# Performance work log

Measured on AMD Instinct MI355X. Metric: run time of the kernel, lower is better.

## Reference

```python
import jax, jax.numpy as jnp
import numpy as np

B = 8192          # batch
NUM_PROTOS = 10   # num_prototypes
NUM_CLASSES = 10
N_PATCHES = 14 * 14  # 196 non-overlapping 2x2 patches of a 28x28 image


def setup_inputs() -> dict:
    key = jax.random.key(0)
    k1, k2, k3 = jax.random.split(key, 3)
    x = jax.random.normal(k1, (B, 784), dtype=jnp.float32)
    prototypes = jax.random.normal(k2, (NUM_PROTOS, 4), dtype=jnp.float32)
    W = jax.random.normal(k3, (NUM_CLASSES, NUM_PROTOS * N_PATCHES), dtype=jnp.float32) * 0.02
    b = jnp.zeros((NUM_CLASSES,), dtype=jnp.float32)
    return {"x": x, "prototypes": prototypes, "W": W, "b": b}


def _features(x, prototypes):
    # x: (B, 784) -> non-overlapping 2x2 patches, row-major within each patch
    bsz = x.shape[0]
    img = x.reshape(bsz, 28, 28)
    patches = img.reshape(bsz, 14, 2, 14, 2).transpose(0, 1, 3, 2, 4).reshape(bsz, N_PATCHES, 4)
    # Quantum kernel: ansatz applies RY(x_i) then RY(-y_i) per wire on |0000>.
    # |0...0> amplitude factorizes over the 4 wires: prod_i cos((x_i - y_i)/2).
    diff = patches[:, :, None, :] - prototypes[None, None, :, :]   # (B, 196, P, 4)
    kern = jnp.abs(jnp.prod(jnp.cos(0.5 * diff), axis=-1))          # (B, 196, P)
    # torch stacks per-prototype then permutes to (B, P, 196) and flattens
    return kern.transpose(0, 2, 1).reshape(bsz, -1)                 # (B, P*196)


def reference(x, prototypes, W, b):
    feats = _features(x, prototypes)
    logits = feats @ W.T + b
    return jax.nn.log_softmax(logits, axis=-1)
```

## Files before the change

kernel.cpp:

```cpp
#include <hip/hip_runtime.h>
#include <math.h>

#define B_ROWS 8192
#define NPROTO 10
#define NCLS   10
#define NPATCH 196
#define WROW   (NPROTO * NPATCH)

#define PART_OFF  0
#define XS_STRIDE 113

typedef float v2f __attribute__((ext_vector_type(2)));

__global__ __launch_bounds__(256) void quanv_main(
    const float* __restrict__ x, const float* __restrict__ protos,
    const float* __restrict__ W, float* __restrict__ partial) {
  __shared__ float xs[64 * XS_STRIDE];
  __shared__ float tbl[80];

  const int tid = threadIdx.x;
  const int bx  = blockIdx.x;
  const int pr2 = blockIdx.y;

  if (tid < 80) {
    int proto = tid >> 3, j = tid & 7;
    float h = 0.5f * protos[proto * 4 + (j & 3)];
    tbl[tid] = (j < 4) ? __cosf(h) : __sinf(h);
  }

  {
    const float* src = x + (size_t)bx * 64 * 784 + pr2 * 112;
    for (int i = tid; i < 64 * 28; i += 256) {
      int row = i / 28, quad = i - row * 28;
      float4 v = *(const float4*)(src + (size_t)row * 784 + quad * 4);
      float* d = &xs[row * XS_STRIDE + quad * 4];
      d[0] = v.x; d[1] = v.y; d[2] = v.z; d[3] = v.w;
    }
  }
  __syncthreads();

  const int wid  = __builtin_amdgcn_readfirstlane(tid >> 6);
  const int lane = tid & 63;
  const float* xr = &xs[lane * XS_STRIDE];
  const int p0 = pr2 * 28 + wid * 7;

  v2f cv01[7], cv23[7], sv01[7], sv23[7];
#pragma unroll
  for (int j = 0; j < 7; ++j) {
    int lp  = wid * 7 + j;
    int piL = lp >= 14 ? 1 : 0;
    int pj  = lp - piL * 14;
    int off = piL * 56 + 2 * pj;
    float x0 = xr[off],      x1 = xr[off + 1];
    float x2 = xr[off + 28], x3 = xr[off + 29];
    float s0, c0, s1, c1, s2, c2, s3, c3;
    __sincosf(0.5f * x0, &s0, &c0);
    __sincosf(0.5f * x1, &s1, &c1);
    __sincosf(0.5f * x2, &s2, &c2);
    __sincosf(0.5f * x3, &s3, &c3);
    cv01[j] = (v2f){c0, c1}; cv23[j] = (v2f){c2, c3};
    sv01[j] = (v2f){s0, s1}; sv23[j] = (v2f){s2, s3};
  }

  v2f acc2[5];
#pragma unroll
  for (int k = 0; k < 5; ++k) acc2[k] = (v2f){0.0f, 0.0f};

#pragma unroll
  for (int proto = 0; proto < NPROTO; ++proto) {
    float4 tc = *(const float4*)&tbl[proto * 8];
    float4 ts = *(const float4*)&tbl[proto * 8 + 4];
    v2f tc01 = {tc.x, tc.y}, tc23 = {tc.z, tc.w};
    v2f ts01 = {ts.x, ts.y}, ts23 = {ts.z, ts.w};
    const float* wbase = W + proto * NPATCH + p0;
#pragma unroll
    for (int j = 0; j < 7; ++j) {
      v2f t01 = __builtin_elementwise_fma(cv01[j], tc01, sv01[j] * ts01);
      v2f t23 = __builtin_elementwise_fma(cv23[j], tc23, sv23[j] * ts23);
      float q = fabsf((t01.x * t01.y) * (t23.x * t23.y));
      v2f qq = {q, q};
      const float* wq = wbase + j;
#pragma unroll
      for (int k = 0; k < 5; ++k) {
        v2f wv = {wq[(2 * k) * WROW], wq[(2 * k + 1) * WROW]};
        acc2[k] = __builtin_elementwise_fma(qq, wv, acc2[k]);
      }
    }
  }

  __syncthreads();
  {
    float* myred = &xs[(wid * 64 + lane) * 11];
#pragma unroll
    for (int k = 0; k < 5; ++k) {
      myred[2 * k]     = acc2[k].x;
      myred[2 * k + 1] = acc2[k].y;
    }
  }
  __syncthreads();

  for (int i = tid; i < 64 * NCLS; i += 256) {
    int row = i / NCLS, c = i - row * NCLS;
    int o = row * 11 + c;
    float s = xs[o] + xs[704 + o] + xs[1408 + o] + xs[2112 + o];
    partial[((size_t)pr2 * B_ROWS + (size_t)bx * 64 + row) * NCLS + c] = s;
  }
}

__global__ __launch_bounds__(256) void quanv_final(
    const float* __restrict__ partial, const float* __restrict__ bias,
    float* __restrict__ out) {
  int r = blockIdx.x * 256 + threadIdx.x;
  float v[NCLS];
#pragma unroll
  for (int c = 0; c < NCLS; c += 2) {
    float2 bb = *(const float2*)(bias + c);
    v[c] = bb.x; v[c + 1] = bb.y;
  }
  for (int y = 0; y < 7; ++y) {
    const float* pp = partial + ((size_t)y * B_ROWS + r) * NCLS;
#pragma unroll
    for (int c = 0; c < NCLS; c += 2) {
      float2 t = *(const float2*)(pp + c);
      v[c] += t.x; v[c + 1] += t.y;
    }
  }
  float m = v[0];
#pragma unroll
  for (int c = 1; c < NCLS; ++c) m = fmaxf(m, v[c]);
  float sum = 0.0f;
#pragma unroll
  for (int c = 0; c < NCLS; ++c) sum += __expf(v[c] - m);
  float lse = m + __logf(sum);
#pragma unroll
  for (int c = 0; c < NCLS; c += 2) {
    float2 o = {v[c] - lse, v[c + 1] - lse};
    *(float2*)(out + (size_t)r * NCLS + c) = o;
  }
}

extern "C" void kernel_launch(void* const* d_in, const int* in_sizes, int n_in,
                              void* d_out, int out_size, void* d_ws, size_t ws_size,
                              hipStream_t stream) {
  const float* x      = (const float*)d_in[0];
  const float* protos = (const float*)d_in[1];
  const float* W      = (const float*)d_in[2];
  const float* bias   = (const float*)d_in[3];
  float* out = (float*)d_out;
  float* ws  = (float*)d_ws;

  quanv_main<<<dim3(B_ROWS / 64, 7), 256, 0, stream>>>(x, protos, W, ws + PART_OFF);
  quanv_final<<<B_ROWS / 256, 256, 0, stream>>>(ws + PART_OFF, bias, out);
}
```

Baseline: 91.81 us.

## Pre-transpose W into padded class-major slab and stage it in LDS

Adds a prep kernel that transposes W into a patch-proto-class layout padded to 12 classes and precomputes the prototype cos/sin table. The main kernel copies its 28-patch slab of this layout into shared memory and reads weights as float4/float2 vectors instead of ten strided scalar global loads per feature. This is meant to cut scattered global and scalar loads in the inner loop. The cost is an extra kernel launch, about 13 KB more LDS per block (which may lower occupancy), and a bulk LDS fill per block.

```diff
diff --git a/kernel.cpp b/kernel.cpp
--- a/kernel.cpp
+++ b/kernel.cpp
@@ -5,28 +5,45 @@
 #define NPROTO 10
 #define NCLS   10
 #define NPATCH 196
-#define WROW   (NPROTO * NPATCH)
+#define WPAD   12
 
-#define PART_OFF  0
+#define TABLE_OFF 0
+#define WT2_OFF   128
+#define PART_OFF  (128 + NPATCH * NPROTO * WPAD)
 #define XS_STRIDE 113
 
 typedef float v2f __attribute__((ext_vector_type(2)));
 
+__global__ __launch_bounds__(256) void quanv_prep(
+    const float* __restrict__ W, const float* __restrict__ protos,
+    float* __restrict__ ws) {
+  int idx = blockIdx.x * 256 + threadIdx.x;
+  if (idx < NPROTO * 8) {
+    int proto = idx >> 3, j = idx & 7;
+    float h = 0.5f * protos[proto * 4 + (j & 3)];
+    ws[TABLE_OFF + idx] = (j < 4) ? __cosf(h) : __sinf(h);
+  }
+  if (idx < NPATCH * NPROTO * WPAD) {
+    int p     = idx / (NPROTO * WPAD);
+    int rem   = idx - p * (NPROTO * WPAD);
+    int proto = rem / WPAD;
+    int c     = rem - proto * WPAD;
+    ws[WT2_OFF + idx] =
+        (c < NCLS) ? W[c * (NPROTO * NPATCH) + proto * NPATCH + p] : 0.0f;
+  }
+}
+
 __global__ __launch_bounds__(256) void quanv_main(
-    const float* __restrict__ x, const float* __restrict__ protos,
-    const float* __restrict__ W, float* __restrict__ partial) {
+    const float* __restrict__ x, const float* __restrict__ ws,
+    float* __restrict__ partial) {
   __shared__ float xs[64 * XS_STRIDE];
+  __shared__ float wslab[28 * NPROTO * WPAD];
   __shared__ float tbl[80];
 
   const int tid = threadIdx.x;
   const int bx  = blockIdx.x;
   const int pr2 = blockIdx.y;
-
-  if (tid < 80) {
-    int proto = tid >> 3, j = tid & 7;
-    float h = 0.5f * protos[proto * 4 + (j & 3)];
-    tbl[tid] = (j < 4) ? __cosf(h) : __sinf(h);
-  }
+  const int p0  = pr2 * 28;
 
   {
     const float* src = x + (size_t)bx * 64 * 784 + pr2 * 112;
@@ -37,12 +54,17 @@
       d[0] = v.x; d[1] = v.y; d[2] = v.z; d[3] = v.w;
     }
   }
+  {
+    const float4* src = (const float4*)(ws + WT2_OFF + p0 * NPROTO * WPAD);
+    float4* dst = (float4*)wslab;
+    for (int i = tid; i < 840; i += 256) dst[i] = src[i];
+  }
+  if (tid < 20) ((float4*)tbl)[tid] = ((const float4*)(ws + TABLE_OFF))[tid];
   __syncthreads();
 
   const int wid  = __builtin_amdgcn_readfirstlane(tid >> 6);
   const int lane = tid & 63;
   const float* xr = &xs[lane * XS_STRIDE];
-  const int p0 = pr2 * 28 + wid * 7;
 
   v2f cv01[7], cv23[7], sv01[7], sv23[7];
 #pragma unroll
@@ -72,19 +94,21 @@
     float4 ts = *(const float4*)&tbl[proto * 8 + 4];
     v2f tc01 = {tc.x, tc.y}, tc23 = {tc.z, tc.w};
     v2f ts01 = {ts.x, ts.y}, ts23 = {ts.z, ts.w};
-    const float* wbase = W + proto * NPATCH + p0;
 #pragma unroll
     for (int j = 0; j < 7; ++j) {
       v2f t01 = __builtin_elementwise_fma(cv01[j], tc01, sv01[j] * ts01);
       v2f t23 = __builtin_elementwise_fma(cv23[j], tc23, sv23[j] * ts23);
       float q = fabsf((t01.x * t01.y) * (t23.x * t23.y));
       v2f qq = {q, q};
-      const float* wq = wbase + j;
-#pragma unroll
-      for (int k = 0; k < 5; ++k) {
-        v2f wv = {wq[(2 * k) * WROW], wq[(2 * k + 1) * WROW]};
-        acc2[k] = __builtin_elementwise_fma(qq, wv, acc2[k]);
-      }
+      const float* wq = &wslab[(wid * 7 + j) * (NPROTO * WPAD) + proto * WPAD];
+      float4 wA = *(const float4*)(wq);
+      float4 wB = *(const float4*)(wq + 4);
+      float2 wC = *(const float2*)(wq + 8);
+      acc2[0] = __builtin_elementwise_fma(qq, (v2f){wA.x, wA.y}, acc2[0]);
+      acc2[1] = __builtin_elementwise_fma(qq, (v2f){wA.z, wA.w}, acc2[1]);
+      acc2[2] = __builtin_elementwise_fma(qq, (v2f){wB.x, wB.y}, acc2[2]);
+      acc2[3] = __builtin_elementwise_fma(qq, (v2f){wB.z, wB.w}, acc2[3]);
+      acc2[4] = __builtin_elementwise_fma(qq, (v2f){wC.x, wC.y}, acc2[4]);
     }
   }
 
@@ -149,6 +173,7 @@
   float* out = (float*)d_out;
   float* ws  = (float*)d_ws;
 
-  quanv_main<<<dim3(B_ROWS / 64, 7), 256, 0, stream>>>(x, protos, W, ws + PART_OFF);
+  quanv_prep<<<(NPATCH * NPROTO * WPAD + 255) / 256, 256, 0, stream>>>(W, protos, ws);
+  quanv_main<<<dim3(B_ROWS / 64, 7), 256, 0, stream>>>(x, ws, ws + PART_OFF);
   quanv_final<<<B_ROWS / 256, 256, 0, stream>>>(ws + PART_OFF, bias, out);
 }
```

Result: no change. 92.13 us (+0.4%).
